# Performance work log

Measured on AMD Instinct MI355X. Metric: run time of the kernel, lower is better.

## Reference

```python
import jax, jax.numpy as jnp
import numpy as np

B, L, D = 512, 33, 4096
P, K, H = 64, 512, 128  # proj_dim, topk, head hidden
LN_EPS = 1e-5


def setup_inputs() -> dict:
    key = jax.random.key(0)
    ks = jax.random.split(key, 12)
    s = lambda fan_in: 1.0 / np.sqrt(fan_in)
    return {
        "x": jax.random.normal(ks[0], (B, L, D), dtype=jnp.float32),
        "Wp": jax.random.uniform(ks[1], (P, L), jnp.float32, -s(L), s(L)),
        "bp": jax.random.uniform(ks[2], (P,), jnp.float32, -s(L), s(L)),
        "ws": jax.random.uniform(ks[3], (P,), jnp.float32, -s(P), s(P)),
        "bs": jax.random.uniform(ks[4], (), jnp.float32, -s(P), s(P)),
        "gamma": jnp.ones((P,), jnp.float32),
        "beta": jnp.zeros((P,), jnp.float32),
        "W1": jax.random.uniform(ks[5], (H, P), jnp.float32, -s(P), s(P)),
        "b1": jax.random.uniform(ks[6], (H,), jnp.float32, -s(P), s(P)),
        "W2": jax.random.uniform(ks[7], (2, H), jnp.float32, -s(H), s(H)),
        "b2": jax.random.uniform(ks[8], (2,), jnp.float32, -s(H), s(H)),
    }


def reference(x, Wp, bp, ws, bs, gamma, beta, W1, b1, W2, b2):
    # x: (B, L, D) -> per-dim layer trajectories projected to P
    h = jnp.einsum("bld,pl->bdp", x, Wp) + bp           # (B, D, P)
    scores = jnp.einsum("bdp,p->bd", h, ws) + bs         # (B, D)
    topk_scores, topk_idx = jax.lax.top_k(scores, K)     # (B, K)
    w = jax.nn.softmax(topk_scores, axis=-1)             # (B, K)
    topk_h = jnp.take_along_axis(h, topk_idx[:, :, None], axis=1)  # (B, K, P)
    out = jnp.einsum("bkp,bk->bp", topk_h, w)            # (B, P)
    # head: LayerNorm -> Linear -> GELU -> Linear (dropout in eval = identity)
    mu = jnp.mean(out, axis=-1, keepdims=True)
    var = jnp.mean((out - mu) ** 2, axis=-1, keepdims=True)
    z = (out - mu) * jax.lax.rsqrt(var + LN_EPS) * gamma + beta
    z = jax.nn.gelu(z @ W1.T + b1, approximate=False)
    return z @ W2.T + b2                                  # (B, 2)
```

## Files before the change

kernel.cpp:

```cpp
#include <hip/hip_runtime.h>
#include <math.h>

#define NB 512
#define LL 33
#define DD 4096
#define PP 64
#define KK 512
#define HH 128
#define LN_EPS 1e-5f
#define NT 512
#define NW (NT / 64)

__device__ __forceinline__ unsigned fkey(float s) {
    unsigned u = __float_as_uint(s);
    return (u & 0x80000000u) ? ~u : (u | 0x80000000u);
}

__device__ __forceinline__ float waveMax(float v) {
    #pragma unroll
    for (int o = 32; o > 0; o >>= 1) v = fmaxf(v, __shfl_xor(v, o));
    return v;
}
__device__ __forceinline__ float waveSum(float v) {
    #pragma unroll
    for (int o = 32; o > 0; o >>= 1) v += __shfl_xor(v, o);
    return v;
}

__global__ __launch_bounds__(NT, 4) void sda_kernel(
    const float* __restrict__ x,
    const float* __restrict__ Wp, const float* __restrict__ bp,
    const float* __restrict__ ws, const float* __restrict__ bsp,
    const float* __restrict__ gamma, const float* __restrict__ beta,
    const float* __restrict__ W1, const float* __restrict__ b1,
    const float* __restrict__ W2, const float* __restrict__ b2,
    float* __restrict__ out)
{
    __shared__ __align__(16) float s_w[DD];
    __shared__ float s_v[LL];
    __shared__ unsigned s_hist[NW][256];
    __shared__ float s_red[NW];
    __shared__ float s_y[LL];
    __shared__ float s_o[PP];
    __shared__ float s_g[HH];
    __shared__ float s_c, s_m, s_S;
    __shared__ unsigned s_prefix, s_kk, s_ceq;

    const int t = threadIdx.x;
    const int lane = t & 63;
    const int wv = t >> 6;
    const int b = blockIdx.x;
    const float* __restrict__ xb = x + (size_t)b * (LL * DD);

    if (t < LL) {
        float a = 0.f;
        for (int p = 0; p < PP; ++p) a += Wp[p * LL + t] * ws[p];
        s_v[t] = a;
    } else if (t == LL) {
        float a = bsp[0];
        for (int p = 0; p < PP; ++p) a += ws[p] * bp[p];
        s_c = a;
    }
    if (t == 0) { s_prefix = 0u; s_kk = KK; s_ceq = 0u; }
    __syncthreads();

    const float c0 = s_c;
    float4* s_w4 = (float4*)s_w;
    const float4* base = (const float4*)xb;
    float4 pa[4], pb[4];
    #pragma unroll
    for (int s = 0; s < 4; ++s) {
        pa[s] = base[s * 1024 + t];
        pb[s] = base[s * 1024 + t + NT];
    }
    float4 acc0 = make_float4(c0, c0, c0, c0);
    float4 acc1 = acc0;
    #pragma unroll
    for (int l = 0; l < LL; ++l) {
        const int s = l & 3;
        const float4 xa = pa[s];
        const float4 xc = pb[s];
        if (l + 4 < LL) {
            pa[s] = base[(l + 4) * 1024 + t];
            pb[s] = base[(l + 4) * 1024 + t + NT];
        }
        const float vl = s_v[l];
        acc0.x += vl * xa.x; acc0.y += vl * xa.y; acc0.z += vl * xa.z; acc0.w += vl * xa.w;
        acc1.x += vl * xc.x; acc1.y += vl * xc.y; acc1.z += vl * xc.z; acc1.w += vl * xc.w;
    }

    unsigned ukey[8];
    s_w4[t] = acc0;
    s_w4[t + NT] = acc1;
    ukey[0] = fkey(acc0.x); ukey[1] = fkey(acc0.y); ukey[2] = fkey(acc0.z); ukey[3] = fkey(acc0.w);
    ukey[4] = fkey(acc1.x); ukey[5] = fkey(acc1.y); ukey[6] = fkey(acc1.z); ukey[7] = fkey(acc1.w);
    float lmax = fmaxf(fmaxf(fmaxf(acc0.x, acc0.y), fmaxf(acc0.z, acc0.w)),
                       fmaxf(fmaxf(acc1.x, acc1.y), fmaxf(acc1.z, acc1.w)));
    lmax = waveMax(lmax);
    if (lane == 0) s_red[wv] = lmax;
    __syncthreads();
    if (t == 0) {
        float m = s_red[0];
        for (int i = 1; i < NW; ++i) m = fmaxf(m, s_red[i]);
        s_m = m;
    }
    __syncthreads();

    for (int shift = 24; shift >= 0; shift -= 8) {
        for (int i = t; i < NW * 256; i += NT) ((unsigned*)s_hist)[i] = 0u;
        __syncthreads();
        const unsigned pfx = s_prefix;
        const unsigned hm = (shift == 24) ? 0u : (0xFFFFFFFFu << (shift + 8));
        #pragma unroll
        for (int i = 0; i < 8; ++i) {
            const unsigned u = ukey[i];
            if ((u & hm) == pfx)
                atomicAdd(&s_hist[wv][(u >> shift) & 255u], 1u);
        }
        __syncthreads();
        if (t < 64) {
            const int b4 = t * 4;
            unsigned c0b = 0, c1b = 0, c2b = 0, c3b = 0;
            for (int w = 0; w < NW; ++w) {
                c0b += s_hist[w][b4 + 0];
                c1b += s_hist[w][b4 + 1];
                c2b += s_hist[w][b4 + 2];
                c3b += s_hist[w][b4 + 3];
            }
            const unsigned s3 = c3b;
            const unsigned s2 = c2b + s3;
            const unsigned s1 = c1b + s2;
            const unsigned s0 = c0b + s1;
            unsigned inc = s0;
            #pragma unroll
            for (int off = 1; off < 64; off <<= 1) {
                const int src = t + off;
                const unsigned other = __shfl(inc, (src < 64) ? src : t);
                inc += (src < 64) ? other : 0u;
            }
            const unsigned excl = inc - s0;
            const unsigned kk = s_kk;
            const unsigned cm0 = excl + s0, cm1 = excl + s1,
                           cm2 = excl + s2, cm3 = excl + s3;
            if (cm0 >= kk && cm0 - c0b < kk) {
                s_prefix = pfx | ((unsigned)(b4 + 0) << shift);
                s_kk = kk - (cm0 - c0b); s_ceq = c0b;
            }
            if (cm1 >= kk && cm1 - c1b < kk) {
                s_prefix = pfx | ((unsigned)(b4 + 1) << shift);
                s_kk = kk - (cm1 - c1b); s_ceq = c1b;
            }
            if (cm2 >= kk && cm2 - c2b < kk) {
                s_prefix = pfx | ((unsigned)(b4 + 2) << shift);
                s_kk = kk - (cm2 - c2b); s_ceq = c2b;
            }
            if (cm3 >= kk && cm3 - c3b < kk) {
                s_prefix = pfx | ((unsigned)(b4 + 3) << shift);
                s_kk = kk - (cm3 - c3b); s_ceq = c3b;
            }
        }
        __syncthreads();
    }
    const unsigned T = s_prefix;
    const unsigned need_eq = s_kk;
    const unsigned count_eq = s_ceq;
    const float m = s_m;

    if (count_eq == need_eq) {
        float4 w0, w1;
        w0.x = (ukey[0] >= T) ? expf(acc0.x - m) : 0.f;
        w0.y = (ukey[1] >= T) ? expf(acc0.y - m) : 0.f;
        w0.z = (ukey[2] >= T) ? expf(acc0.z - m) : 0.f;
        w0.w = (ukey[3] >= T) ? expf(acc0.w - m) : 0.f;
        w1.x = (ukey[4] >= T) ? expf(acc1.x - m) : 0.f;
        w1.y = (ukey[5] >= T) ? expf(acc1.y - m) : 0.f;
        w1.z = (ukey[6] >= T) ? expf(acc1.z - m) : 0.f;
        w1.w = (ukey[7] >= T) ? expf(acc1.w - m) : 0.f;
        s_w4[t] = w0;
        s_w4[t + NT] = w1;
        float lsum = w0.x + w0.y + w0.z + w0.w + w1.x + w1.y + w1.z + w1.w;
        lsum = waveSum(lsum);
        if (lane == 0) s_red[wv] = lsum;
        __syncthreads();
        if (t == 0) {
            float S = 0.f;
            for (int i = 0; i < NW; ++i) S += s_red[i];
            s_S = S;
        }
        __syncthreads();
    } else {
        __syncthreads();
        if (t == 0) {
            unsigned taken = 0;
            float S = 0.f;
            for (int d = 0; d < DD; ++d) {
                const float s = s_w[d];
                const unsigned u = fkey(s);
                float w = 0.f;
                if (u > T) w = expf(s - m);
                else if (u == T && taken < need_eq) { w = expf(s - m); ++taken; }
                s_w[d] = w;
                S += w;
            }
            s_S = S;
        }
        __syncthreads();
    }
    const float invS = 1.0f / s_S;

    for (int k = 4; k >= 0; --k) {
        const int l = wv + NW * k;
        if (l < LL) {
            const float4* row = (const float4*)(xb + l * DD);
            float a = 0.f;
            #pragma unroll
            for (int j = 15; j >= 0; --j) {
                const int f = lane + j * 64;
                const float4 xv = row[f];
                const float4 w4 = s_w4[f];
                a += w4.x * xv.x + w4.y * xv.y + w4.z * xv.z + w4.w * xv.w;
            }
            a = waveSum(a);
            if (lane == 0) s_y[l] = a;
        }
    }
    __syncthreads();

    if (t < PP) {
        float a = 0.f;
        for (int l = 0; l < LL; ++l) a += Wp[t * LL + l] * s_y[l];
        s_o[t] = a * invS + bp[t];
    }
    __syncthreads();
    if (wv == 0) {
        const float o = s_o[lane];
        const float mu = waveSum(o) * (1.f / PP);
        const float dv = o - mu;
        const float var = waveSum(dv * dv) * (1.f / PP);
        s_o[lane] = dv * rsqrtf(var + LN_EPS) * gamma[lane] + beta[lane];
    }
    __syncthreads();
    if (t < HH) {
        float a = b1[t];
        for (int p = 0; p < PP; ++p) a += W1[t * PP + p] * s_o[p];
        s_g[t] = 0.5f * a * (1.f + erff(a * 0.70710678118654752440f));
    }
    __syncthreads();
    if (t < 2) {
        float a = b2[t];
        for (int j = 0; j < HH; ++j) a += W2[t * HH + j] * s_g[j];
        out[b * 2 + t] = a;
    }
}

extern "C" void kernel_launch(void* const* d_in, const int* in_sizes, int n_in,
                              void* d_out, int out_size, void* d_ws, size_t ws_size,
                              hipStream_t stream) {
    const float* x     = (const float*)d_in[0];
    const float* Wp    = (const float*)d_in[1];
    const float* bp    = (const float*)d_in[2];
    const float* ws    = (const float*)d_in[3];
    const float* bs    = (const float*)d_in[4];
    const float* gamma = (const float*)d_in[5];
    const float* beta  = (const float*)d_in[6];
    const float* W1    = (const float*)d_in[7];
    const float* b1    = (const float*)d_in[8];
    const float* W2    = (const float*)d_in[9];
    const float* b2    = (const float*)d_in[10];
    float* out = (float*)d_out;
    hipLaunchKernelGGL(sda_kernel, dim3(NB), dim3(NT), 0, stream,
                       x, Wp, bp, ws, bs, gamma, beta, W1, b1, W2, b2, out);
}
```

Measured before the change: 414.1 us.

## Keep softmax weights in registers and compute layer dot-products with prefetched per-thread loads

```diff
diff --git a/kernel.cpp b/kernel.cpp
--- a/kernel.cpp
+++ b/kernel.cpp
@@ -40,6 +40,7 @@
     __shared__ float s_v[LL];
     __shared__ unsigned s_hist[NW][256];
     __shared__ float s_red[NW];
+    __shared__ float s_yp[NW][LL];
     __shared__ float s_y[LL];
     __shared__ float s_o[PP];
     __shared__ float s_g[HH];
@@ -166,8 +167,9 @@
     const unsigned count_eq = s_ceq;
     const float m = s_m;
 
-    if (count_eq == need_eq) {
-        float4 w0, w1;
+    float4 w0, w1;
+    const bool rare = (count_eq != need_eq);
+    if (!rare) {
         w0.x = (ukey[0] >= T) ? expf(acc0.x - m) : 0.f;
         w0.y = (ukey[1] >= T) ? expf(acc0.y - m) : 0.f;
         w0.z = (ukey[2] >= T) ? expf(acc0.z - m) : 0.f;
@@ -176,8 +178,6 @@
         w1.y = (ukey[5] >= T) ? expf(acc1.y - m) : 0.f;
         w1.z = (ukey[6] >= T) ? expf(acc1.z - m) : 0.f;
         w1.w = (ukey[7] >= T) ? expf(acc1.w - m) : 0.f;
-        s_w4[t] = w0;
-        s_w4[t + NT] = w1;
         float lsum = w0.x + w0.y + w0.z + w0.w + w1.x + w1.y + w1.z + w1.w;
         lsum = waveSum(lsum);
         if (lane == 0) s_red[wv] = lsum;
@@ -189,7 +189,6 @@
         }
         __syncthreads();
     } else {
-        __syncthreads();
         if (t == 0) {
             unsigned taken = 0;
             float S = 0.f;
@@ -205,24 +204,41 @@
             s_S = S;
         }
         __syncthreads();
+        w0 = s_w4[t];
+        w1 = s_w4[t + NT];
     }
     const float invS = 1.0f / s_S;
 
-    for (int k = 4; k >= 0; --k) {
-        const int l = wv + NW * k;
-        if (l < LL) {
-            const float4* row = (const float4*)(xb + l * DD);
-            float a = 0.f;
-            #pragma unroll
-            for (int j = 15; j >= 0; --j) {
-                const int f = lane + j * 64;
-                const float4 xv = row[f];
-                const float4 w4 = s_w4[f];
-                a += w4.x * xv.x + w4.y * xv.y + w4.z * xv.z + w4.w * xv.w;
-            }
-            a = waveSum(a);
-            if (lane == 0) s_y[l] = a;
-        }
+    float yloc[LL];
+    float4 qa[4], qb[4];
+    #pragma unroll
+    for (int s = 0; s < 4; ++s) {
+        qa[s] = base[(LL - 1 - s) * 1024 + t];
+        qb[s] = base[(LL - 1 - s) * 1024 + t + NT];
+    }
+    #pragma unroll
+    for (int i = 0; i < LL; ++i) {
+        const int l = LL - 1 - i;
+        const int s = i & 3;
+        const float4 xa = qa[s];
+        const float4 xc = qb[s];
+        if (i + 4 < LL) {
+            qa[s] = base[(LL - 1 - (i + 4)) * 1024 + t];
+            qb[s] = base[(LL - 1 - (i + 4)) * 1024 + t + NT];
+        }
+        yloc[l] = w0.x * xa.x + w0.y * xa.y + w0.z * xa.z + w0.w * xa.w
+                + w1.x * xc.x + w1.y * xc.y + w1.z * xc.z + w1.w * xc.w;
+    }
+    #pragma unroll
+    for (int l = 0; l < LL; ++l) {
+        const float v = waveSum(yloc[l]);
+        if (lane == 0) s_yp[wv][l] = v;
+    }
+    __syncthreads();
+    if (t < LL) {
+        float a = 0.f;
+        for (int w = 0; w < NW; ++w) a += s_yp[w][t];
+        s_y[t] = a;
     }
     __syncthreads();
 
```

Result: slower. 528.5 us (+27.6%).
